# Optimization experiments

Hardware: AMD Instinct MI355X
Metric: run time of the kernel (lower is better)

Reference implementation:

```python
import jax, jax.numpy as jnp
import numpy as np

N_FULL = 200000  # full-graph nodes
N_SUB = 80000    # subgraph nodes
E = 800000       # subgraph edges
IN = 128         # input feature dim
HD = 128         # hidden dim
LMAX = 5         # max ACT depth


def setup_inputs() -> dict:
    key = jax.random.key(0)
    ks = jax.random.split(key, 12)
    s = lambda i, shape: jax.random.normal(ks[i], shape, jnp.float32) * 0.05
    return dict(
        x_full=jax.random.normal(ks[0], (N_FULL, IN), jnp.float32),
        W_in=s(1, (HD, IN)), b_in=jnp.zeros((HD,), jnp.float32),
        W_l=s(2, (HD, HD)), b_l=jnp.zeros((HD,), jnp.float32),
        W_r=s(3, (HD, HD)),
        W_e1=s(4, (HD, 3 * HD)), b_e1=jnp.zeros((HD,), jnp.float32),
        W_e2=s(5, (1, HD)), b_e2=jnp.zeros((1,), jnp.float32),
        W_h1=s(6, (64, 2 * HD + 1)), b_h1=jnp.zeros((64,), jnp.float32),
        W_h2=s(7, (1, 64)), b_h2=jnp.zeros((1,), jnp.float32),
        subset=jax.random.randint(ks[8], (N_SUB,), 0, N_FULL),
        edge_index=jax.random.randint(ks[9], (2, E), 0, N_SUB),
    )


def reference(x_full, W_in, b_in, W_l, b_l, W_r, W_e1, b_e1, W_e2, b_e2,
              W_h1, b_h1, W_h2, b_h2, subset, edge_index):
    src, dst = edge_index[0], edge_index[1]
    # in-degree for mean aggregation (PyG SAGEConv default aggr='mean')
    deg = jax.ops.segment_sum(jnp.ones((E,), x_full.dtype), dst, num_segments=N_SUB)
    deg = jnp.maximum(deg, 1.0)[:, None]

    def sage_step(Hn):
        agg = jax.ops.segment_sum(Hn[src], dst, num_segments=N_SUB) / deg
        return jax.nn.relu(agg @ W_l.T + b_l + Hn @ W_r.T)

    # input projection of gathered subgraph features
    Hk = x_full[subset] @ W_in.T + b_in
    u_idx, v_idx = 0, 1  # mapping of (u, v) in relabeled subgraph

    alphas, scores = [], []
    p_not = jnp.float32(1.0)
    for depth_k in range(1, LMAX + 1):
        # incremental: one more shared SAGE step == k fresh steps from H0
        Hk = sage_step(Hk)
        h_u, h_v = Hk[u_idx], Hk[v_idx]
        feat = jnp.concatenate([h_u, h_v, h_u * h_v])            # [3*HD]
        score = jax.nn.relu(feat @ W_e1.T + b_e1) @ W_e2.T + b_e2  # [1]
        hin = jnp.concatenate([h_u, h_v, score])                  # [2*HD+1]
        p_halt = jax.nn.sigmoid(jax.nn.relu(hin @ W_h1.T + b_h1) @ W_h2.T + b_h2)[0]
        alphas.append(p_halt * p_not)
        scores.append(score[0])
        p_not = p_not * (1.0 - p_halt)

    alpha = jnp.stack(alphas)
    alpha = alpha / (alpha.sum() + 1e-8)
    scores_v = jnp.stack(scores)
    final_score = (alpha * scores_v).sum()
    depths = jnp.arange(1, LMAX + 1, dtype=jnp.float32)
    expected_depth = (alpha * depths).sum()
    return final_score, expected_depth, alpha
```

## Files before the change

### kernel.cpp

```cpp
#include <hip/hip_runtime.h>
#include <hip/hip_bf16.h>

#define N_FULL 200000
#define N_SUB  80000
#define E_NUM  800000
#define IN_DIM 128
#define HD     128
#define LMAX   5

#define NB_SCAN ((N_SUB + 255) / 256)


__global__ void init_all(int* __restrict__ cnt, int* __restrict__ cursor,
                         int* __restrict__ level) {
    int i = blockIdx.x * blockDim.x + threadIdx.x;
    if (i < N_SUB) {
        cnt[i] = 0;
        cursor[i] = 0;
        level[i] = (i < 2) ? 0 : 7;
    }
}

__global__ void count_deg(const int* __restrict__ dst, int* __restrict__ cnt) {
    int i = blockIdx.x * blockDim.x + threadIdx.x;
    if (i < E_NUM) atomicAdd(&cnt[dst[i]], 1);
}

__global__ void scan_block(const int* __restrict__ cnt, int* __restrict__ offs,
                           int* __restrict__ bsums) {
    __shared__ int s[256];
    int t = threadIdx.x;
    int i = blockIdx.x * 256 + t;
    int v = (i < N_SUB) ? cnt[i] : 0;
    s[t] = v;
    __syncthreads();
    for (int off = 1; off < 256; off <<= 1) {
        int x = (t >= off) ? s[t - off] : 0;
        __syncthreads();
        s[t] += x;
        __syncthreads();
    }
    if (i < N_SUB) offs[i] = s[t] - v;
    if (t == 255) bsums[blockIdx.x] = s[255];
}

__global__ void scan_sums(int* __restrict__ bsums) {
    __shared__ int s[512];
    int t = threadIdx.x;
    int v = (t < NB_SCAN) ? bsums[t] : 0;
    s[t] = v;
    __syncthreads();
    for (int off = 1; off < 512; off <<= 1) {
        int x = (t >= off) ? s[t - off] : 0;
        __syncthreads();
        s[t] += x;
        __syncthreads();
    }
    if (t < NB_SCAN) bsums[t] = s[t] - v;
}

__global__ void scan_add(int* __restrict__ offs, const int* __restrict__ bsums) {
    int i = blockIdx.x * 256 + threadIdx.x;
    if (i < N_SUB) offs[i] += bsums[blockIdx.x];
    if (i == 0) offs[N_SUB] = E_NUM;
}

__global__ void fill_csr(const int* __restrict__ src, const int* __restrict__ dst,
                         const int* __restrict__ offs, int* __restrict__ cursor,
                         int* __restrict__ csr) {
    int i = blockIdx.x * blockDim.x + threadIdx.x;
    if (i < E_NUM) {
        int d = dst[i];
        int p = atomicAdd(&cursor[d], 1);
        csr[offs[d] + p] = src[i];
    }
}


__global__ void bfs_csr(const int* __restrict__ offs, const int* __restrict__ csr,
                        int* __restrict__ level, int t) {
    int i = blockIdx.x * blockDim.x + threadIdx.x;
    if (i >= N_SUB) return;
    if (level[i] != t) return;
    int beg = offs[i], end = offs[i + 1];
    for (int j = beg; j < end; ++j) {
        int u = csr[j];
        if (level[u] > t + 1) level[u] = t + 1;
    }
}


__global__ __launch_bounds__(256) void hist_levels(const int* __restrict__ level,
                                                   int* __restrict__ bhist) {
    __shared__ int h[8];
    int t = threadIdx.x;
    if (t < 8) h[t] = 0;
    __syncthreads();
    int i = blockIdx.x * 256 + t;
    if (i < N_SUB) {
        int l = level[i];
        if (l > 5) l = 6;
        atomicAdd(&h[l], 1);
    }
    __syncthreads();
    if (t < 8) bhist[blockIdx.x * 8 + t] = h[t];
}

__global__ void scan_hist(int* __restrict__ bhist, int* __restrict__ base,
                          int* __restrict__ cum) {
    __shared__ int tot[8];
    int t = threadIdx.x;
    if (t < 8) {
        int acc = 0;
        for (int b = 0; b < NB_SCAN; ++b) {
            int v = bhist[b * 8 + t];
            bhist[b * 8 + t] = acc;
            acc += v;
        }
        tot[t] = acc;
    }
    __syncthreads();
    if (t == 0) {
        int acc = 0;
        for (int l = 0; l <= 5; ++l) {
            base[l] = acc;
            acc += tot[l];
            cum[l] = acc;
        }
    }
}

__global__ __launch_bounds__(256) void emit_order(const int* __restrict__ level,
                                                  const int* __restrict__ bhist,
                                                  const int* __restrict__ base,
                                                  int* __restrict__ order) {
    __shared__ int woff[4][8];
    int t = threadIdx.x;
    int lane = t & 63, wv = t >> 6;
    int i = blockIdx.x * 256 + t;
    int l = 7;
    if (i < N_SUB) {
        l = level[i];
        if (l > 5) l = 6;
    }
    unsigned long long mybal = 0;
#pragma unroll
    for (int q = 0; q < 8; ++q) {
        unsigned long long b = __ballot(l == q);
        if (q == l) mybal = b;
        if (lane == 0) woff[wv][q] = (int)__popcll(b);
    }
    int inrank = (int)__popcll(mybal & ((1ull << lane) - 1ull));
    __syncthreads();
    if (t < 8) {
        int acc = 0;
        for (int w2 = 0; w2 < 4; ++w2) {
            int c = woff[w2][t];
            woff[w2][t] = acc;
            acc += c;
        }
    }
    __syncthreads();
    if (i < N_SUB && l <= 5) {
        int pos = base[l] + bhist[blockIdx.x * 8 + l] + woff[wv][l] + inrank;
        order[pos] = i;
    }
}


__global__ __launch_bounds__(256) void wcomb(
    const float* __restrict__ W_l, const float* __restrict__ W_r,
    const float* __restrict__ W_in, const float* __restrict__ b_in,
    const float* __restrict__ b_l, float* __restrict__ Wc1,
    float* __restrict__ Wc2, float* __restrict__ bc) {
    int f = blockIdx.x;
    int t = threadIdx.x;
    int c = t & 127, p = t >> 7;
    __shared__ float wl[128], wr[128];
    if (t < 128) wl[t] = W_l[f * 128 + t];
    else wr[t - 128] = W_r[f * 128 + (t - 128)];
    __syncthreads();
    const float* wrow = p ? wr : wl;
    float acc = 0.f;
#pragma unroll 8
    for (int j = 0; j < 128; ++j)
        acc = fmaf(wrow[j], W_in[j * 128 + c], acc);
    (p ? Wc2 : Wc1)[f * 128 + c] = acc;
    if (t < 64) {
        float pa = (wl[t] + wr[t]) * b_in[t] + (wl[t + 64] + wr[t + 64]) * b_in[t + 64];
        for (int off = 32; off; off >>= 1) pa += __shfl_down(pa, off);
        if (t == 0) bc[f] = pa + b_l[f];
    }
}


__global__ __launch_bounds__(256) void aggregate_list(
    const float* __restrict__ H, float* __restrict__ Out,
    const int* __restrict__ offs, const int* __restrict__ csr,
    const int* __restrict__ cnt, const int* __restrict__ order,
    const int* __restrict__ cumptr, int lvl, const int* __restrict__ srcmap) {
    int M = cumptr[lvl];
    int ngroups = (M + 3) >> 2;
    int wid = threadIdx.x >> 6, lane = threadIdx.x & 63;
    for (int g = blockIdx.x; g < ngroups; g += gridDim.x) {
        int ni = g * 4 + wid;
        if (ni >= M) continue;
        int node = order[ni];
        int beg = offs[node], end = offs[node + 1];
        float ax = 0.f, ay = 0.f, bx = 0.f, by = 0.f;
        int j = beg;
        for (; j + 1 < end; j += 2) {
            int s0 = csr[j], s1 = csr[j + 1];
            int r0 = srcmap ? srcmap[s0] : s0;
            int r1 = srcmap ? srcmap[s1] : s1;
            float2 v0 = *(const float2*)(H + (size_t)r0 * HD + lane * 2);
            float2 v1 = *(const float2*)(H + (size_t)r1 * HD + lane * 2);
            ax += v0.x; ay += v0.y;
            bx += v1.x; by += v1.y;
        }
        if (j < end) {
            int s0 = csr[j];
            int r0 = srcmap ? srcmap[s0] : s0;
            float2 v0 = *(const float2*)(H + (size_t)r0 * HD + lane * 2);
            ax += v0.x; ay += v0.y;
        }
        int c = cnt[node];
        float inv = 1.0f / (float)(c > 1 ? c : 1);
        *(float2*)(Out + (size_t)node * HD + lane * 2) =
            make_float2((ax + bx) * inv, (ay + by) * inv);
    }
}


#define GBM 64
#define GBK 32

__global__ __launch_bounds__(256) void gemm_list(
    const float* __restrict__ A1, const float* __restrict__ A2,
    const float* __restrict__ W1, const float* __restrict__ W2,
    const float* __restrict__ bias, float* __restrict__ Out,
    const int* __restrict__ order, const int* __restrict__ gatherA,
    const int* __restrict__ gatherB, const int* __restrict__ cumptr,
    int lvl, int do_relu) {

    __shared__ __align__(16) float As[GBK][68];
    __shared__ __align__(16) float Ws[GBK][132];

    int M = cumptr[lvl];
    int ntiles = (M + GBM - 1) / GBM;
    int tid = threadIdx.x;
    int tx = tid & 15, ty = tid >> 4;
    int r0 = ty * 4;
    int c0 = tx * 4;
    int nchunk = A2 ? 8 : 4;

    for (int tile = blockIdx.x; tile < ntiles; tile += gridDim.x) {
        int row0 = tile * GBM;

        float acc[4][8];
#pragma unroll
        for (int i = 0; i < 4; ++i)
#pragma unroll
            for (int j = 0; j < 8; ++j) acc[i][j] = 0.f;

        for (int ch = 0; ch < nchunk; ++ch) {
            const float* Asrc = (ch < 4) ? A1 : A2;
            const float* Wsrc = (ch < 4) ? W1 : W2;
            const int* gmap = (ch < 4) ? gatherA : gatherB;
            int kbase = (ch & 3) * GBK;

#pragma unroll
            for (int it = 0; it < 2; ++it) {
                int idx = tid + it * 256;
                int m = idx >> 3, kq = idx & 7;
                int row = row0 + m;
                float4 v = make_float4(0.f, 0.f, 0.f, 0.f);
                if (row < M) {
                    int nr = order[row];
                    int ar = gmap ? gmap[nr] : nr;
                    v = *(const float4*)(Asrc + (size_t)ar * 128 + kbase + kq * 4);
                }
                As[kq * 4 + 0][m] = v.x;
                As[kq * 4 + 1][m] = v.y;
                As[kq * 4 + 2][m] = v.z;
                As[kq * 4 + 3][m] = v.w;
            }
#pragma unroll
            for (int it = 0; it < 4; ++it) {
                int idx = tid + it * 256;
                int n = idx >> 3, kq = idx & 7;
                float4 v = *(const float4*)(Wsrc + n * 128 + kbase + kq * 4);
                Ws[kq * 4 + 0][n] = v.x;
                Ws[kq * 4 + 1][n] = v.y;
                Ws[kq * 4 + 2][n] = v.z;
                Ws[kq * 4 + 3][n] = v.w;
            }
            __syncthreads();

#pragma unroll
            for (int kk = 0; kk < GBK; ++kk) {
                float4 a  = *(const float4*)&As[kk][r0];
                float4 w0 = *(const float4*)&Ws[kk][c0];
                float4 w1 = *(const float4*)&Ws[kk][c0 + 64];
                float av[4] = {a.x, a.y, a.z, a.w};
                float wv[8] = {w0.x, w0.y, w0.z, w0.w, w1.x, w1.y, w1.z, w1.w};
#pragma unroll
                for (int i = 0; i < 4; ++i)
#pragma unroll
                    for (int j = 0; j < 8; ++j)
                        acc[i][j] = fmaf(av[i], wv[j], acc[i][j]);
            }
            __syncthreads();
        }

#pragma unroll
        for (int i = 0; i < 4; ++i) {
            int row = row0 + r0 + i;
            if (row >= M) continue;
            int nr = order[row];
            float4 o0, o1;
            o0.x = acc[i][0] + bias[c0 + 0];
            o0.y = acc[i][1] + bias[c0 + 1];
            o0.z = acc[i][2] + bias[c0 + 2];
            o0.w = acc[i][3] + bias[c0 + 3];
            o1.x = acc[i][4] + bias[c0 + 64];
            o1.y = acc[i][5] + bias[c0 + 65];
            o1.z = acc[i][6] + bias[c0 + 66];
            o1.w = acc[i][7] + bias[c0 + 67];
            if (do_relu) {
                o0.x = fmaxf(o0.x, 0.f); o0.y = fmaxf(o0.y, 0.f);
                o0.z = fmaxf(o0.z, 0.f); o0.w = fmaxf(o0.w, 0.f);
                o1.x = fmaxf(o1.x, 0.f); o1.y = fmaxf(o1.y, 0.f);
                o1.z = fmaxf(o1.z, 0.f); o1.w = fmaxf(o1.w, 0.f);
            }
            *(float4*)(Out + (size_t)nr * 128 + c0) = o0;
            *(float4*)(Out + (size_t)nr * 128 + c0 + 64) = o1;
        }
    }
}


__global__ __launch_bounds__(256) void head_kernel(
    const float* __restrict__ H,
    const float* __restrict__ W_e1, const float* __restrict__ b_e1,
    const float* __restrict__ W_e2, const float* __restrict__ b_e2,
    const float* __restrict__ W_h1, const float* __restrict__ b_h1,
    const float* __restrict__ W_h2, const float* __restrict__ b_h2,
    float* __restrict__ head_out, int kidx) {

    __shared__ float feat[384];
    __shared__ float rowo[128];
    __shared__ float sc_sh;
    int t = threadIdx.x, lane = t & 63, wv = t >> 6;

    if (t < 128) {
        float a = H[t], b = H[128 + t];
        feat[t] = a;
        feat[128 + t] = b;
        feat[256 + t] = a * b;
    }
    __syncthreads();

    for (int r = wv; r < 128; r += 4) {
        const float* wr = W_e1 + r * 384;
        float acc = 0.f;
#pragma unroll
        for (int j = 0; j < 6; ++j)
            acc += feat[lane + 64 * j] * wr[lane + 64 * j];
        for (int off = 32; off; off >>= 1) acc += __shfl_down(acc, off);
        if (lane == 0) rowo[r] = fmaxf(acc + b_e1[r], 0.f) * W_e2[r];
    }
    __syncthreads();
    if (wv == 0) {
        float v = rowo[lane] + rowo[lane + 64];
        for (int off = 32; off; off >>= 1) v += __shfl_down(v, off);
        if (lane == 0) sc_sh = v + b_e2[0];
    }
    __syncthreads();
    float score = sc_sh;

    for (int r = wv; r < 64; r += 4) {
        const float* wh = W_h1 + r * 257;
        float acc = 0.f;
#pragma unroll
        for (int j = 0; j < 4; ++j)
            acc += feat[lane + 64 * j] * wh[lane + 64 * j];
        if (lane == 0) acc += score * wh[256];
        for (int off = 32; off; off >>= 1) acc += __shfl_down(acc, off);
        if (lane == 0) rowo[r] = fmaxf(acc + b_h1[r], 0.f) * W_h2[r];
    }
    __syncthreads();
    if (wv == 0) {
        float v = rowo[lane];
        for (int off = 32; off; off >>= 1) v += __shfl_down(v, off);
        if (lane == 0) {
            float p = 1.f / (1.f + expf(-(v + b_h2[0])));
            head_out[kidx * 2 + 0] = score;
            head_out[kidx * 2 + 1] = p;
        }
    }
}

__global__ void finalize(const float* __restrict__ head_out, float* __restrict__ out) {
    if (threadIdx.x == 0 && blockIdx.x == 0) {
        float a[LMAX];
        float p_not = 1.f, s = 0.f;
        for (int k = 0; k < LMAX; ++k) {
            float p = head_out[2 * k + 1];
            a[k] = p * p_not;
            p_not *= (1.f - p);
            s += a[k];
        }
        float inv = 1.f / (s + 1e-8f);
        float fs = 0.f, ed = 0.f;
        for (int k = 0; k < LMAX; ++k) {
            float al = a[k] * inv;
            out[2 + k] = al;
            fs += al * head_out[2 * k];
            ed += al * (float)(k + 1);
        }
        out[0] = fs;
        out[1] = ed;
    }
}


extern "C" void kernel_launch(void* const* d_in, const int* in_sizes, int n_in,
                              void* d_out, int out_size, void* d_ws, size_t ws_size,
                              hipStream_t stream) {
    const float* x_full = (const float*)d_in[0];
    const float* W_in  = (const float*)d_in[1];
    const float* b_in  = (const float*)d_in[2];
    const float* W_l   = (const float*)d_in[3];
    const float* b_l   = (const float*)d_in[4];
    const float* W_r   = (const float*)d_in[5];
    const float* W_e1  = (const float*)d_in[6];
    const float* b_e1  = (const float*)d_in[7];
    const float* W_e2  = (const float*)d_in[8];
    const float* b_e2  = (const float*)d_in[9];
    const float* W_h1  = (const float*)d_in[10];
    const float* b_h1  = (const float*)d_in[11];
    const float* W_h2  = (const float*)d_in[12];
    const float* b_h2  = (const float*)d_in[13];
    const int* subset  = (const int*)d_in[14];
    const int* edge    = (const int*)d_in[15];
    const int* esrc = edge;
    const int* edst = edge + E_NUM;

    char* w = (char*)d_ws;
    float* HA = (float*)w;      w += (size_t)N_SUB * HD * 4;
    float* HB = (float*)w;      w += (size_t)N_SUB * HD * 4;
    int* cnt = (int*)w;         w += (size_t)N_SUB * 4;
    int* offs = (int*)w;        w += (size_t)(N_SUB + 64) * 4;
    int* cursor = (int*)w;      w += (size_t)N_SUB * 4;
    int* csr = (int*)w;         w += (size_t)E_NUM * 4;
    int* level = (int*)w;       w += (size_t)N_SUB * 4;
    int* order = (int*)w;       w += (size_t)N_SUB * 4;
    int* bsums = (int*)w;       w += 4096;
    int* bhist = (int*)w;       w += (size_t)(NB_SCAN + 1) * 8 * 4;
    int* lvlbase = (int*)w;     w += 64;
    int* cum = (int*)w;         w += 64;
    float* Wc1 = (float*)w;     w += 128 * 128 * 4;
    float* Wc2 = (float*)w;     w += 128 * 128 * 4;
    float* bc = (float*)w;      w += 512;
    float* head_out = (float*)w; w += 256;

    init_all<<<NB_SCAN, 256, 0, stream>>>(cnt, cursor, level);
    count_deg<<<(E_NUM + 255) / 256, 256, 0, stream>>>(edst, cnt);
    scan_block<<<NB_SCAN, 256, 0, stream>>>(cnt, offs, bsums);
    scan_sums<<<1, 512, 0, stream>>>(bsums);
    scan_add<<<NB_SCAN, 256, 0, stream>>>(offs, bsums);
    fill_csr<<<(E_NUM + 255) / 256, 256, 0, stream>>>(esrc, edst, offs, cursor, csr);

    wcomb<<<128, 256, 0, stream>>>(W_l, W_r, W_in, b_in, b_l, Wc1, Wc2, bc);

    for (int t = 0; t < 4; ++t)
        bfs_csr<<<NB_SCAN, 256, 0, stream>>>(offs, csr, level, t);

    hist_levels<<<NB_SCAN, 256, 0, stream>>>(level, bhist);
    scan_hist<<<1, 64, 0, stream>>>(bhist, lvlbase, cum);
    emit_order<<<NB_SCAN, 256, 0, stream>>>(level, bhist, lvlbase, order);

    aggregate_list<<<2048, 256, 0, stream>>>(x_full, HB, offs, csr, cnt, order, cum, 4, subset);
    gemm_list<<<512, 256, 0, stream>>>(
        HB, x_full, Wc1, Wc2, bc, HA, order, nullptr, subset, cum, 4, 1);
    head_kernel<<<1, 256, 0, stream>>>(HA, W_e1, b_e1, W_e2, b_e2,
                                       W_h1, b_h1, W_h2, b_h2, head_out, 0);

    for (int k = 2; k <= LMAX; ++k) {
        int lvl = LMAX - k;
        aggregate_list<<<96, 256, 0, stream>>>(HA, HB, offs, csr, cnt, order, cum, lvl, nullptr);
        gemm_list<<<96, 256, 0, stream>>>(
            HB, HA, W_l, W_r, b_l, HA, order, nullptr, nullptr, cum, lvl, 1);
        head_kernel<<<1, 256, 0, stream>>>(HA, W_e1, b_e1, W_e2, b_e2,
                                           W_h1, b_h1, W_h2, b_h2, head_out, k - 1);
    }
    finalize<<<1, 1, 0, stream>>>(head_out, (float*)d_out);
}
```

Before: 449.7 us.

## Fuse preprocessing and tail stages into persistent kernels with grid barriers

```diff
diff --git a/kernel.cpp b/kernel.cpp
--- a/kernel.cpp
+++ b/kernel.cpp
@@ -9,200 +9,32 @@
 #define LMAX   5
 
 #define NB_SCAN ((N_SUB + 255) / 256)
-
-
-__global__ void init_all(int* __restrict__ cnt, int* __restrict__ cursor,
-                         int* __restrict__ level) {
-    int i = blockIdx.x * blockDim.x + threadIdx.x;
-    if (i < N_SUB) {
-        cnt[i] = 0;
-        cursor[i] = 0;
-        level[i] = (i < 2) ? 0 : 7;
-    }
-}
-
-__global__ void count_deg(const int* __restrict__ dst, int* __restrict__ cnt) {
-    int i = blockIdx.x * blockDim.x + threadIdx.x;
-    if (i < E_NUM) atomicAdd(&cnt[dst[i]], 1);
-}
-
-__global__ void scan_block(const int* __restrict__ cnt, int* __restrict__ offs,
-                           int* __restrict__ bsums) {
-    __shared__ int s[256];
-    int t = threadIdx.x;
-    int i = blockIdx.x * 256 + t;
-    int v = (i < N_SUB) ? cnt[i] : 0;
-    s[t] = v;
-    __syncthreads();
-    for (int off = 1; off < 256; off <<= 1) {
-        int x = (t >= off) ? s[t - off] : 0;
-        __syncthreads();
-        s[t] += x;
-        __syncthreads();
-    }
-    if (i < N_SUB) offs[i] = s[t] - v;
-    if (t == 255) bsums[blockIdx.x] = s[255];
-}
-
-__global__ void scan_sums(int* __restrict__ bsums) {
-    __shared__ int s[512];
-    int t = threadIdx.x;
-    int v = (t < NB_SCAN) ? bsums[t] : 0;
-    s[t] = v;
-    __syncthreads();
-    for (int off = 1; off < 512; off <<= 1) {
-        int x = (t >= off) ? s[t - off] : 0;
-        __syncthreads();
-        s[t] += x;
-        __syncthreads();
-    }
-    if (t < NB_SCAN) bsums[t] = s[t] - v;
-}
-
-__global__ void scan_add(int* __restrict__ offs, const int* __restrict__ bsums) {
-    int i = blockIdx.x * 256 + threadIdx.x;
-    if (i < N_SUB) offs[i] += bsums[blockIdx.x];
-    if (i == 0) offs[N_SUB] = E_NUM;
-}
-
-__global__ void fill_csr(const int* __restrict__ src, const int* __restrict__ dst,
-                         const int* __restrict__ offs, int* __restrict__ cursor,
-                         int* __restrict__ csr) {
-    int i = blockIdx.x * blockDim.x + threadIdx.x;
-    if (i < E_NUM) {
-        int d = dst[i];
-        int p = atomicAdd(&cursor[d], 1);
-        csr[offs[d] + p] = src[i];
-    }
-}
-
-
-__global__ void bfs_csr(const int* __restrict__ offs, const int* __restrict__ csr,
-                        int* __restrict__ level, int t) {
-    int i = blockIdx.x * blockDim.x + threadIdx.x;
-    if (i >= N_SUB) return;
-    if (level[i] != t) return;
-    int beg = offs[i], end = offs[i + 1];
-    for (int j = beg; j < end; ++j) {
-        int u = csr[j];
-        if (level[u] > t + 1) level[u] = t + 1;
-    }
-}
-
-
-__global__ __launch_bounds__(256) void hist_levels(const int* __restrict__ level,
-                                                   int* __restrict__ bhist) {
-    __shared__ int h[8];
-    int t = threadIdx.x;
-    if (t < 8) h[t] = 0;
-    __syncthreads();
-    int i = blockIdx.x * 256 + t;
-    if (i < N_SUB) {
-        int l = level[i];
-        if (l > 5) l = 6;
-        atomicAdd(&h[l], 1);
-    }
-    __syncthreads();
-    if (t < 8) bhist[blockIdx.x * 8 + t] = h[t];
-}
-
-__global__ void scan_hist(int* __restrict__ bhist, int* __restrict__ base,
-                          int* __restrict__ cum) {
-    __shared__ int tot[8];
-    int t = threadIdx.x;
-    if (t < 8) {
-        int acc = 0;
-        for (int b = 0; b < NB_SCAN; ++b) {
-            int v = bhist[b * 8 + t];
-            bhist[b * 8 + t] = acc;
-            acc += v;
-        }
-        tot[t] = acc;
-    }
-    __syncthreads();
-    if (t == 0) {
-        int acc = 0;
-        for (int l = 0; l <= 5; ++l) {
-            base[l] = acc;
-            acc += tot[l];
-            cum[l] = acc;
-        }
-    }
-}
-
-__global__ __launch_bounds__(256) void emit_order(const int* __restrict__ level,
-                                                  const int* __restrict__ bhist,
-                                                  const int* __restrict__ base,
-                                                  int* __restrict__ order) {
-    __shared__ int woff[4][8];
-    int t = threadIdx.x;
-    int lane = t & 63, wv = t >> 6;
-    int i = blockIdx.x * 256 + t;
-    int l = 7;
-    if (i < N_SUB) {
-        l = level[i];
-        if (l > 5) l = 6;
-    }
-    unsigned long long mybal = 0;
-#pragma unroll
-    for (int q = 0; q < 8; ++q) {
-        unsigned long long b = __ballot(l == q);
-        if (q == l) mybal = b;
-        if (lane == 0) woff[wv][q] = (int)__popcll(b);
-    }
-    int inrank = (int)__popcll(mybal & ((1ull << lane) - 1ull));
-    __syncthreads();
-    if (t < 8) {
-        int acc = 0;
-        for (int w2 = 0; w2 < 4; ++w2) {
-            int c = woff[w2][t];
-            woff[w2][t] = acc;
-            acc += c;
-        }
-    }
-    __syncthreads();
-    if (i < N_SUB && l <= 5) {
-        int pos = base[l] + bhist[blockIdx.x * 8 + l] + woff[wv][l] + inrank;
-        order[pos] = i;
-    }
-}
-
-
-__global__ __launch_bounds__(256) void wcomb(
-    const float* __restrict__ W_l, const float* __restrict__ W_r,
-    const float* __restrict__ W_in, const float* __restrict__ b_in,
-    const float* __restrict__ b_l, float* __restrict__ Wc1,
-    float* __restrict__ Wc2, float* __restrict__ bc) {
-    int f = blockIdx.x;
-    int t = threadIdx.x;
-    int c = t & 127, p = t >> 7;
-    __shared__ float wl[128], wr[128];
-    if (t < 128) wl[t] = W_l[f * 128 + t];
-    else wr[t - 128] = W_r[f * 128 + (t - 128)];
-    __syncthreads();
-    const float* wrow = p ? wr : wl;
-    float acc = 0.f;
-#pragma unroll 8
-    for (int j = 0; j < 128; ++j)
-        acc = fmaf(wrow[j], W_in[j * 128 + c], acc);
-    (p ? Wc2 : Wc1)[f * 128 + c] = acc;
-    if (t < 64) {
-        float pa = (wl[t] + wr[t]) * b_in[t] + (wl[t + 64] + wr[t + 64]) * b_in[t + 64];
-        for (int off = 32; off; off >>= 1) pa += __shfl_down(pa, off);
-        if (t == 0) bc[f] = pa + b_l[f];
-    }
-}
-
-
-__global__ __launch_bounds__(256) void aggregate_list(
+#define NBP 128
+#define NBT 128
+
+
+__device__ __forceinline__ void gbar(int* bar, int nblk, int ph) {
+    __syncthreads();
+    if (threadIdx.x == 0) {
+        __threadfence();
+        atomicAdd(bar, 1);
+        int target = nblk * ph;
+        while (__hip_atomic_load(bar, __ATOMIC_ACQUIRE, __HIP_MEMORY_SCOPE_AGENT) < target) {
+            __builtin_amdgcn_s_sleep(1);
+        }
+    }
+    __syncthreads();
+}
+
+
+__device__ void dev_aggregate(
     const float* __restrict__ H, float* __restrict__ Out,
     const int* __restrict__ offs, const int* __restrict__ csr,
     const int* __restrict__ cnt, const int* __restrict__ order,
-    const int* __restrict__ cumptr, int lvl, const int* __restrict__ srcmap) {
-    int M = cumptr[lvl];
+    int M, const int* __restrict__ srcmap, int bid0, int nb) {
     int ngroups = (M + 3) >> 2;
     int wid = threadIdx.x >> 6, lane = threadIdx.x & 63;
-    for (int g = blockIdx.x; g < ngroups; g += gridDim.x) {
+    for (int g = bid0; g < ngroups; g += nb) {
         int ni = g * 4 + wid;
         if (ni >= M) continue;
         int node = order[ni];
@@ -231,22 +63,19 @@
     }
 }
 
-
 #define GBM 64
 #define GBK 32
 
-__global__ __launch_bounds__(256) void gemm_list(
+__device__ void dev_gemm(
     const float* __restrict__ A1, const float* __restrict__ A2,
     const float* __restrict__ W1, const float* __restrict__ W2,
     const float* __restrict__ bias, float* __restrict__ Out,
     const int* __restrict__ order, const int* __restrict__ gatherA,
-    const int* __restrict__ gatherB, const int* __restrict__ cumptr,
-    int lvl, int do_relu) {
+    const int* __restrict__ gatherB, int M, int do_relu, int bid0, int nb) {
 
     __shared__ __align__(16) float As[GBK][68];
     __shared__ __align__(16) float Ws[GBK][132];
 
-    int M = cumptr[lvl];
     int ntiles = (M + GBM - 1) / GBM;
     int tid = threadIdx.x;
     int tx = tid & 15, ty = tid >> 4;
@@ -254,7 +83,7 @@
     int c0 = tx * 4;
     int nchunk = A2 ? 8 : 4;
 
-    for (int tile = blockIdx.x; tile < ntiles; tile += gridDim.x) {
+    for (int tile = bid0; tile < ntiles; tile += nb) {
         int row0 = tile * GBM;
 
         float acc[4][8];
@@ -339,8 +168,7 @@
     }
 }
 
-
-__global__ __launch_bounds__(256) void head_kernel(
+__device__ void dev_head(
     const float* __restrict__ H,
     const float* __restrict__ W_e1, const float* __restrict__ b_e1,
     const float* __restrict__ W_e2, const float* __restrict__ b_e2,
@@ -399,10 +227,260 @@
             head_out[kidx * 2 + 1] = p;
         }
     }
-}
-
-__global__ void finalize(const float* __restrict__ head_out, float* __restrict__ out) {
-    if (threadIdx.x == 0 && blockIdx.x == 0) {
+    __syncthreads();
+}
+
+
+__global__ __launch_bounds__(256) void prep_fused(
+    const int* __restrict__ esrc, const int* __restrict__ edst,
+    const float* __restrict__ W_l, const float* __restrict__ W_r,
+    const float* __restrict__ W_in, const float* __restrict__ b_in,
+    const float* __restrict__ b_l,
+    int* __restrict__ cnt, int* __restrict__ cursor, int* __restrict__ level,
+    int* __restrict__ offs, int* __restrict__ csr,
+    int* __restrict__ bsums, int* __restrict__ bhist,
+    int* __restrict__ lvlbase, int* __restrict__ cum, int* __restrict__ order,
+    float* __restrict__ Wc1, float* __restrict__ Wc2, float* __restrict__ bc,
+    int* __restrict__ bar) {
+
+    __shared__ int si[256];
+    __shared__ float sf[256];
+    __shared__ int h8[8];
+    __shared__ int tot8[8];
+    __shared__ int woff[4][8];
+
+    int t = threadIdx.x;
+    int bid = blockIdx.x;
+    int nb = gridDim.x;
+    int gsz = nb * 256;
+    int gi0 = bid * 256 + t;
+    int ph = 0;
+
+    for (int i = gi0; i < N_SUB; i += gsz) {
+        cnt[i] = 0; cursor[i] = 0; level[i] = (i < 2) ? 0 : 7;
+    }
+    gbar(bar, nb, ++ph);
+
+    for (int i = gi0; i < E_NUM; i += gsz)
+        atomicAdd(&cnt[edst[i]], 1);
+    gbar(bar, nb, ++ph);
+
+    for (int job = bid; job < NB_SCAN; job += nb) {
+        int i = job * 256 + t;
+        int v = (i < N_SUB) ? cnt[i] : 0;
+        si[t] = v;
+        __syncthreads();
+        for (int off = 1; off < 256; off <<= 1) {
+            int x = (t >= off) ? si[t - off] : 0;
+            __syncthreads();
+            si[t] += x;
+            __syncthreads();
+        }
+        if (i < N_SUB) offs[i] = si[t] - v;
+        if (t == 255) bsums[job] = si[255];
+        __syncthreads();
+    }
+    gbar(bar, nb, ++ph);
+
+    if (bid == 0 && t < 64) {
+        int lane = t;
+        int base = 0;
+        for (int c = 0; c < NB_SCAN; c += 64) {
+            int idx = c + lane;
+            int v0 = (idx < NB_SCAN) ? bsums[idx] : 0;
+            int v = v0;
+            for (int off = 1; off < 64; off <<= 1) {
+                int x = __shfl_up(v, off);
+                if (lane >= off) v += x;
+            }
+            if (idx < NB_SCAN) bsums[idx] = base + v - v0;
+            base += __shfl(v, 63);
+        }
+    }
+    gbar(bar, nb, ++ph);
+
+    for (int i = gi0; i < N_SUB; i += gsz) offs[i] += bsums[i >> 8];
+    if (gi0 == 0) offs[N_SUB] = E_NUM;
+    gbar(bar, nb, ++ph);
+
+    for (int i = gi0; i < E_NUM; i += gsz) {
+        int d = edst[i];
+        int p = atomicAdd(&cursor[d], 1);
+        csr[offs[d] + p] = esrc[i];
+    }
+    gbar(bar, nb, ++ph);
+
+    for (int tt = 0; tt < 4; ++tt) {
+        for (int i = gi0; i < N_SUB; i += gsz) {
+            if (level[i] == tt) {
+                int beg = offs[i], end = offs[i + 1];
+                for (int j = beg; j < end; ++j) {
+                    int u = csr[j];
+                    if (level[u] > tt + 1) level[u] = tt + 1;
+                }
+            }
+        }
+        gbar(bar, nb, ++ph);
+    }
+
+    for (int job = bid; job < NB_SCAN; job += nb) {
+        if (t < 8) h8[t] = 0;
+        __syncthreads();
+        int i = job * 256 + t;
+        if (i < N_SUB) {
+            int l = level[i];
+            if (l > 5) l = 6;
+            atomicAdd(&h8[l], 1);
+        }
+        __syncthreads();
+        if (t < 8) bhist[job * 8 + t] = h8[t];
+        __syncthreads();
+    }
+    gbar(bar, nb, ++ph);
+
+    if (bid == 0) {
+        int wv = t >> 6, lane = t & 63;
+        for (int l = wv; l < 8; l += 4) {
+            int base = 0;
+            for (int c = 0; c < NB_SCAN; c += 64) {
+                int idx = c + lane;
+                int v0 = (idx < NB_SCAN) ? bhist[idx * 8 + l] : 0;
+                int v = v0;
+                for (int off = 1; off < 64; off <<= 1) {
+                    int x = __shfl_up(v, off);
+                    if (lane >= off) v += x;
+                }
+                if (idx < NB_SCAN) bhist[idx * 8 + l] = base + v - v0;
+                base += __shfl(v, 63);
+            }
+            if (lane == 0) tot8[l] = base;
+        }
+        __syncthreads();
+        if (t == 0) {
+            int acc = 0;
+            for (int l = 0; l <= 5; ++l) {
+                lvlbase[l] = acc;
+                acc += tot8[l];
+                cum[l] = acc;
+            }
+        }
+    }
+    gbar(bar, nb, ++ph);
+
+    {
+        int lane = t & 63, wv = t >> 6;
+        for (int job = bid; job < NB_SCAN; job += nb) {
+            int i = job * 256 + t;
+            int l = 7;
+            if (i < N_SUB) {
+                l = level[i];
+                if (l > 5) l = 6;
+            }
+            unsigned long long mybal = 0;
+#pragma unroll
+            for (int q = 0; q < 8; ++q) {
+                unsigned long long b = __ballot(l == q);
+                if (q == l) mybal = b;
+                if (lane == 0) woff[wv][q] = (int)__popcll(b);
+            }
+            int inrank = (int)__popcll(mybal & ((1ull << lane) - 1ull));
+            __syncthreads();
+            if (t < 8) {
+                int acc = 0;
+                for (int w2 = 0; w2 < 4; ++w2) {
+                    int c = woff[w2][t];
+                    woff[w2][t] = acc;
+                    acc += c;
+                }
+            }
+            __syncthreads();
+            if (i < N_SUB && l <= 5) {
+                int pos = lvlbase[l] + bhist[job * 8 + l] + woff[wv][l] + inrank;
+                order[pos] = i;
+            }
+            __syncthreads();
+        }
+    }
+
+    for (int f = bid; f < 128; f += nb) {
+        if (t < 128) sf[t] = W_l[f * 128 + t];
+        else sf[t] = W_r[f * 128 + (t - 128)];
+        __syncthreads();
+        int c = t & 127, p = t >> 7;
+        const float* wrow = p ? (sf + 128) : sf;
+        float acc = 0.f;
+#pragma unroll 8
+        for (int j = 0; j < 128; ++j)
+            acc = fmaf(wrow[j], W_in[j * 128 + c], acc);
+        (p ? Wc2 : Wc1)[f * 128 + c] = acc;
+        if (t < 64) {
+            float pa = (sf[t] + sf[128 + t]) * b_in[t] +
+                       (sf[t + 64] + sf[192 + t]) * b_in[t + 64];
+            for (int off = 32; off; off >>= 1) pa += __shfl_down(pa, off);
+            if (t == 0) bc[f] = pa + b_l[f];
+        }
+        __syncthreads();
+    }
+}
+
+
+__global__ __launch_bounds__(256) void aggregate_list(
+    const float* __restrict__ H, float* __restrict__ Out,
+    const int* __restrict__ offs, const int* __restrict__ csr,
+    const int* __restrict__ cnt, const int* __restrict__ order,
+    const int* __restrict__ cumptr, int lvl, const int* __restrict__ srcmap) {
+    int M = cumptr[lvl];
+    dev_aggregate(H, Out, offs, csr, cnt, order, M, srcmap, blockIdx.x, gridDim.x);
+}
+
+__global__ __launch_bounds__(256) void gemm_list(
+    const float* __restrict__ A1, const float* __restrict__ A2,
+    const float* __restrict__ W1, const float* __restrict__ W2,
+    const float* __restrict__ bias, float* __restrict__ Out,
+    const int* __restrict__ order, const int* __restrict__ gatherA,
+    const int* __restrict__ gatherB, const int* __restrict__ cumptr,
+    int lvl, int do_relu) {
+    int M = cumptr[lvl];
+    dev_gemm(A1, A2, W1, W2, bias, Out, order, gatherA, gatherB, M, do_relu,
+             blockIdx.x, gridDim.x);
+}
+
+
+__global__ __launch_bounds__(256) void tail_fused(
+    float* __restrict__ HA, float* __restrict__ HB,
+    const int* __restrict__ offs, const int* __restrict__ csr,
+    const int* __restrict__ cnt, const int* __restrict__ order,
+    const int* __restrict__ cum,
+    const float* __restrict__ W_l, const float* __restrict__ b_l,
+    const float* __restrict__ W_r,
+    const float* __restrict__ W_e1, const float* __restrict__ b_e1,
+    const float* __restrict__ W_e2, const float* __restrict__ b_e2,
+    const float* __restrict__ W_h1, const float* __restrict__ b_h1,
+    const float* __restrict__ W_h2, const float* __restrict__ b_h2,
+    float* __restrict__ head_out, float* __restrict__ out,
+    int* __restrict__ bar) {
+
+    int bid = blockIdx.x, nb = gridDim.x;
+    int ph = 0;
+
+    if (bid == 0)
+        dev_head(HA, W_e1, b_e1, W_e2, b_e2, W_h1, b_h1, W_h2, b_h2, head_out, 0);
+    gbar(bar, nb, ++ph);
+
+    for (int k = 2; k <= LMAX; ++k) {
+        int lvl = LMAX - k;
+        int M = cum[lvl];
+        dev_aggregate(HA, HB, offs, csr, cnt, order, M, nullptr, bid, nb);
+        gbar(bar, nb, ++ph);
+        dev_gemm(HB, HA, W_l, W_r, b_l, HA, order, nullptr, nullptr, M, 1, bid, nb);
+        gbar(bar, nb, ++ph);
+        if (bid == 0)
+            dev_head(HA, W_e1, b_e1, W_e2, b_e2, W_h1, b_h1, W_h2, b_h2,
+                     head_out, k - 1);
+        if (k < LMAX) gbar(bar, nb, ++ph);
+    }
+
+    if (bid == 0 && threadIdx.x == 0) {
         float a[LMAX];
         float p_not = 1.f, s = 0.f;
         for (int k = 0; k < LMAX; ++k) {
@@ -464,36 +542,22 @@
     float* Wc2 = (float*)w;     w += 128 * 128 * 4;
     float* bc = (float*)w;      w += 512;
     float* head_out = (float*)w; w += 256;
-
-    init_all<<<NB_SCAN, 256, 0, stream>>>(cnt, cursor, level);
-    count_deg<<<(E_NUM + 255) / 256, 256, 0, stream>>>(edst, cnt);
-    scan_block<<<NB_SCAN, 256, 0, stream>>>(cnt, offs, bsums);
-    scan_sums<<<1, 512, 0, stream>>>(bsums);
-    scan_add<<<NB_SCAN, 256, 0, stream>>>(offs, bsums);
-    fill_csr<<<(E_NUM + 255) / 256, 256, 0, stream>>>(esrc, edst, offs, cursor, csr);
-
-    wcomb<<<128, 256, 0, stream>>>(W_l, W_r, W_in, b_in, b_l, Wc1, Wc2, bc);
-
-    for (int t = 0; t < 4; ++t)
-        bfs_csr<<<NB_SCAN, 256, 0, stream>>>(offs, csr, level, t);
-
-    hist_levels<<<NB_SCAN, 256, 0, stream>>>(level, bhist);
-    scan_hist<<<1, 64, 0, stream>>>(bhist, lvlbase, cum);
-    emit_order<<<NB_SCAN, 256, 0, stream>>>(level, bhist, lvlbase, order);
-
-    aggregate_list<<<2048, 256, 0, stream>>>(x_full, HB, offs, csr, cnt, order, cum, 4, subset);
+    int* bars = (int*)w;        w += 256;
+
+    hipMemsetAsync(bars, 0, 256, stream);
+
+    prep_fused<<<NBP, 256, 0, stream>>>(
+        esrc, edst, W_l, W_r, W_in, b_in, b_l,
+        cnt, cursor, level, offs, csr, bsums, bhist, lvlbase, cum, order,
+        Wc1, Wc2, bc, bars);
+
+    aggregate_list<<<2048, 256, 0, stream>>>(
+        x_full, HB, offs, csr, cnt, order, cum, 4, subset);
     gemm_list<<<512, 256, 0, stream>>>(
         HB, x_full, Wc1, Wc2, bc, HA, order, nullptr, subset, cum, 4, 1);
-    head_kernel<<<1, 256, 0, stream>>>(HA, W_e1, b_e1, W_e2, b_e2,
-                                       W_h1, b_h1, W_h2, b_h2, head_out, 0);
-
-    for (int k = 2; k <= LMAX; ++k) {
-        int lvl = LMAX - k;
-        aggregate_list<<<96, 256, 0, stream>>>(HA, HB, offs, csr, cnt, order, cum, lvl, nullptr);
-        gemm_list<<<96, 256, 0, stream>>>(
-            HB, HA, W_l, W_r, b_l, HA, order, nullptr, nullptr, cum, lvl, 1);
-        head_kernel<<<1, 256, 0, stream>>>(HA, W_e1, b_e1, W_e2, b_e2,
-                                           W_h1, b_h1, W_h2, b_h2, head_out, k - 1);
-    }
-    finalize<<<1, 1, 0, stream>>>(head_out, (float*)d_out);
-}
+
+    tail_fused<<<NBT, 256, 0, stream>>>(
+        HA, HB, offs, csr, cnt, order, cum,
+        W_l, b_l, W_r, W_e1, b_e1, W_e2, b_e2, W_h1, b_h1, W_h2, b_h2,
+        head_out, (float*)d_out, bars + 16);
+}
```

Measured after the change: 855.8 us. 1.9x slower.

## Fuse setup kernels, CSR fill with weight combine, and head into GEMM

Applied to the files above, without the earlier changes.

```diff
diff --git a/kernel.cpp b/kernel.cpp
--- a/kernel.cpp
+++ b/kernel.cpp
@@ -9,22 +9,15 @@
 #define LMAX   5
 
 #define NB_SCAN ((N_SUB + 255) / 256)
-
-
-__global__ void init_all(int* __restrict__ cnt, int* __restrict__ cursor,
-                         int* __restrict__ level) {
-    int i = blockIdx.x * blockDim.x + threadIdx.x;
-    if (i < N_SUB) {
-        cnt[i] = 0;
-        cursor[i] = 0;
-        level[i] = (i < 2) ? 0 : 7;
-    }
-}
+#define NB_E (E_NUM / 256)
+#define WCOMB_BLKS 128
+
 
 __global__ void count_deg(const int* __restrict__ dst, int* __restrict__ cnt) {
     int i = blockIdx.x * blockDim.x + threadIdx.x;
     if (i < E_NUM) atomicAdd(&cnt[dst[i]], 1);
 }
+
 
 __global__ void scan_block(const int* __restrict__ cnt, int* __restrict__ offs,
                            int* __restrict__ bsums) {
@@ -59,20 +52,50 @@
     if (t < NB_SCAN) bsums[t] = s[t] - v;
 }
 
-__global__ void scan_add(int* __restrict__ offs, const int* __restrict__ bsums) {
+__global__ void scan_add(int* __restrict__ offs, const int* __restrict__ bsums,
+                         int* __restrict__ level) {
     int i = blockIdx.x * 256 + threadIdx.x;
-    if (i < N_SUB) offs[i] += bsums[blockIdx.x];
+    if (i < N_SUB) {
+        offs[i] += bsums[blockIdx.x];
+        level[i] = (i < 2) ? 0 : 7;
+    }
     if (i == 0) offs[N_SUB] = E_NUM;
 }
 
-__global__ void fill_csr(const int* __restrict__ src, const int* __restrict__ dst,
-                         const int* __restrict__ offs, int* __restrict__ cursor,
-                         int* __restrict__ csr) {
-    int i = blockIdx.x * blockDim.x + threadIdx.x;
-    if (i < E_NUM) {
-        int d = dst[i];
-        int p = atomicAdd(&cursor[d], 1);
-        csr[offs[d] + p] = src[i];
+
+__global__ __launch_bounds__(256) void fill_wcomb(
+    const int* __restrict__ esrc, const int* __restrict__ edst,
+    const int* __restrict__ offs, int* __restrict__ cnt, int* __restrict__ csr,
+    const float* __restrict__ W_l, const float* __restrict__ W_r,
+    const float* __restrict__ W_in, const float* __restrict__ b_in,
+    const float* __restrict__ b_l,
+    float* __restrict__ Wc1, float* __restrict__ Wc2, float* __restrict__ bc) {
+    int b = blockIdx.x;
+    int t = threadIdx.x;
+    if (b < NB_E) {
+        int i = b * 256 + t;
+        int d = edst[i];
+        int p = atomicSub(&cnt[d], 1) - 1;
+        csr[offs[d] + p] = esrc[i];
+    } else {
+        __shared__ float sf[256];
+        int f = b - NB_E;
+        if (t < 128) sf[t] = W_l[f * 128 + t];
+        else sf[t] = W_r[f * 128 + (t - 128)];
+        __syncthreads();
+        int c = t & 127, p = t >> 7;
+        const float* wrow = p ? (sf + 128) : sf;
+        float acc = 0.f;
+#pragma unroll 8
+        for (int j = 0; j < 128; ++j)
+            acc = fmaf(wrow[j], W_in[j * 128 + c], acc);
+        (p ? Wc2 : Wc1)[f * 128 + c] = acc;
+        if (t < 64) {
+            float pa = (sf[t] + sf[128 + t]) * b_in[t] +
+                       (sf[t + 64] + sf[192 + t]) * b_in[t + 64];
+            for (int off = 32; off; off >>= 1) pa += __shfl_down(pa, off);
+            if (t == 0) bc[f] = pa + b_l[f];
+        }
     }
 }
 
@@ -168,38 +191,12 @@
 }
 
 
-__global__ __launch_bounds__(256) void wcomb(
-    const float* __restrict__ W_l, const float* __restrict__ W_r,
-    const float* __restrict__ W_in, const float* __restrict__ b_in,
-    const float* __restrict__ b_l, float* __restrict__ Wc1,
-    float* __restrict__ Wc2, float* __restrict__ bc) {
-    int f = blockIdx.x;
-    int t = threadIdx.x;
-    int c = t & 127, p = t >> 7;
-    __shared__ float wl[128], wr[128];
-    if (t < 128) wl[t] = W_l[f * 128 + t];
-    else wr[t - 128] = W_r[f * 128 + (t - 128)];
-    __syncthreads();
-    const float* wrow = p ? wr : wl;
-    float acc = 0.f;
-#pragma unroll 8
-    for (int j = 0; j < 128; ++j)
-        acc = fmaf(wrow[j], W_in[j * 128 + c], acc);
-    (p ? Wc2 : Wc1)[f * 128 + c] = acc;
-    if (t < 64) {
-        float pa = (wl[t] + wr[t]) * b_in[t] + (wl[t + 64] + wr[t + 64]) * b_in[t + 64];
-        for (int off = 32; off; off >>= 1) pa += __shfl_down(pa, off);
-        if (t == 0) bc[f] = pa + b_l[f];
-    }
-}
-
-
 __global__ __launch_bounds__(256) void aggregate_list(
     const float* __restrict__ H, float* __restrict__ Out,
     const int* __restrict__ offs, const int* __restrict__ csr,
-    const int* __restrict__ cnt, const int* __restrict__ order,
-    const int* __restrict__ cumptr, int lvl, const int* __restrict__ srcmap) {
-    int M = cumptr[lvl];
+    const int* __restrict__ order, const int* __restrict__ cum, int lvl,
+    const int* __restrict__ srcmap) {
+    int M = cum[lvl];
     int ngroups = (M + 3) >> 2;
     int wid = threadIdx.x >> 6, lane = threadIdx.x & 63;
     for (int g = blockIdx.x; g < ngroups; g += gridDim.x) {
@@ -224,11 +221,75 @@
             float2 v0 = *(const float2*)(H + (size_t)r0 * HD + lane * 2);
             ax += v0.x; ay += v0.y;
         }
-        int c = cnt[node];
-        float inv = 1.0f / (float)(c > 1 ? c : 1);
+        int deg = end - beg;
+        float inv = 1.0f / (float)(deg > 1 ? deg : 1);
         *(float2*)(Out + (size_t)node * HD + lane * 2) =
             make_float2((ax + bx) * inv, (ay + by) * inv);
     }
+}
+
+
+__device__ void dev_head(
+    const float* __restrict__ H,
+    const float* __restrict__ W_e1, const float* __restrict__ b_e1,
+    const float* __restrict__ W_e2, const float* __restrict__ b_e2,
+    const float* __restrict__ W_h1, const float* __restrict__ b_h1,
+    const float* __restrict__ W_h2, const float* __restrict__ b_h2,
+    float* __restrict__ head_out, int kidx) {
+
+    __shared__ float feat[384];
+    __shared__ float rowo[128];
+    __shared__ float sc_sh;
+    int t = threadIdx.x, lane = t & 63, wv = t >> 6;
+
+    __syncthreads();
+    if (t < 128) {
+        float a = H[t], b = H[128 + t];
+        feat[t] = a;
+        feat[128 + t] = b;
+        feat[256 + t] = a * b;
+    }
+    __syncthreads();
+
+    for (int r = wv; r < 128; r += 4) {
+        const float* wr = W_e1 + r * 384;
+        float acc = 0.f;
+#pragma unroll
+        for (int j = 0; j < 6; ++j)
+            acc += feat[lane + 64 * j] * wr[lane + 64 * j];
+        for (int off = 32; off; off >>= 1) acc += __shfl_down(acc, off);
+        if (lane == 0) rowo[r] = fmaxf(acc + b_e1[r], 0.f) * W_e2[r];
+    }
+    __syncthreads();
+    if (wv == 0) {
+        float v = rowo[lane] + rowo[lane + 64];
+        for (int off = 32; off; off >>= 1) v += __shfl_down(v, off);
+        if (lane == 0) sc_sh = v + b_e2[0];
+    }
+    __syncthreads();
+    float score = sc_sh;
+
+    for (int r = wv; r < 64; r += 4) {
+        const float* wh = W_h1 + r * 257;
+        float acc = 0.f;
+#pragma unroll
+        for (int j = 0; j < 4; ++j)
+            acc += feat[lane + 64 * j] * wh[lane + 64 * j];
+        if (lane == 0) acc += score * wh[256];
+        for (int off = 32; off; off >>= 1) acc += __shfl_down(acc, off);
+        if (lane == 0) rowo[r] = fmaxf(acc + b_h1[r], 0.f) * W_h2[r];
+    }
+    __syncthreads();
+    if (wv == 0) {
+        float v = rowo[lane];
+        for (int off = 32; off; off >>= 1) v += __shfl_down(v, off);
+        if (lane == 0) {
+            float p = 1.f / (1.f + expf(-(v + b_h2[0])));
+            head_out[kidx * 2 + 0] = score;
+            head_out[kidx * 2 + 1] = p;
+        }
+    }
+    __syncthreads();
 }
 
 
@@ -240,19 +301,22 @@
     const float* __restrict__ W1, const float* __restrict__ W2,
     const float* __restrict__ bias, float* __restrict__ Out,
     const int* __restrict__ order, const int* __restrict__ gatherA,
-    const int* __restrict__ gatherB, const int* __restrict__ cumptr,
-    int lvl, int do_relu) {
+    const int* __restrict__ gatherB, const int* __restrict__ cum, int lvl,
+    const float* __restrict__ W_e1, const float* __restrict__ b_e1,
+    const float* __restrict__ W_e2, const float* __restrict__ b_e2,
+    const float* __restrict__ W_h1, const float* __restrict__ b_h1,
+    const float* __restrict__ W_h2, const float* __restrict__ b_h2,
+    float* __restrict__ head_out, int head_kidx) {
 
     __shared__ __align__(16) float As[GBK][68];
     __shared__ __align__(16) float Ws[GBK][132];
 
-    int M = cumptr[lvl];
+    int M = cum[lvl];
     int ntiles = (M + GBM - 1) / GBM;
     int tid = threadIdx.x;
     int tx = tid & 15, ty = tid >> 4;
     int r0 = ty * 4;
     int c0 = tx * 4;
-    int nchunk = A2 ? 8 : 4;
 
     for (int tile = blockIdx.x; tile < ntiles; tile += gridDim.x) {
         int row0 = tile * GBM;
@@ -263,7 +327,7 @@
 #pragma unroll
             for (int j = 0; j < 8; ++j) acc[i][j] = 0.f;
 
-        for (int ch = 0; ch < nchunk; ++ch) {
+        for (int ch = 0; ch < 8; ++ch) {
             const float* Asrc = (ch < 4) ? A1 : A2;
             const float* Wsrc = (ch < 4) ? W1 : W2;
             const int* gmap = (ch < 4) ? gatherA : gatherB;
@@ -319,87 +383,25 @@
             if (row >= M) continue;
             int nr = order[row];
             float4 o0, o1;
-            o0.x = acc[i][0] + bias[c0 + 0];
-            o0.y = acc[i][1] + bias[c0 + 1];
-            o0.z = acc[i][2] + bias[c0 + 2];
-            o0.w = acc[i][3] + bias[c0 + 3];
-            o1.x = acc[i][4] + bias[c0 + 64];
-            o1.y = acc[i][5] + bias[c0 + 65];
-            o1.z = acc[i][6] + bias[c0 + 66];
-            o1.w = acc[i][7] + bias[c0 + 67];
-            if (do_relu) {
-                o0.x = fmaxf(o0.x, 0.f); o0.y = fmaxf(o0.y, 0.f);
-                o0.z = fmaxf(o0.z, 0.f); o0.w = fmaxf(o0.w, 0.f);
-                o1.x = fmaxf(o1.x, 0.f); o1.y = fmaxf(o1.y, 0.f);
-                o1.z = fmaxf(o1.z, 0.f); o1.w = fmaxf(o1.w, 0.f);
-            }
+            o0.x = fmaxf(acc[i][0] + bias[c0 + 0], 0.f);
+            o0.y = fmaxf(acc[i][1] + bias[c0 + 1], 0.f);
+            o0.z = fmaxf(acc[i][2] + bias[c0 + 2], 0.f);
+            o0.w = fmaxf(acc[i][3] + bias[c0 + 3], 0.f);
+            o1.x = fmaxf(acc[i][4] + bias[c0 + 64], 0.f);
+            o1.y = fmaxf(acc[i][5] + bias[c0 + 65], 0.f);
+            o1.z = fmaxf(acc[i][6] + bias[c0 + 66], 0.f);
+            o1.w = fmaxf(acc[i][7] + bias[c0 + 67], 0.f);
             *(float4*)(Out + (size_t)nr * 128 + c0) = o0;
             *(float4*)(Out + (size_t)nr * 128 + c0 + 64) = o1;
         }
-    }
-}
-
-
-__global__ __launch_bounds__(256) void head_kernel(
-    const float* __restrict__ H,
-    const float* __restrict__ W_e1, const float* __restrict__ b_e1,
-    const float* __restrict__ W_e2, const float* __restrict__ b_e2,
-    const float* __restrict__ W_h1, const float* __restrict__ b_h1,
-    const float* __restrict__ W_h2, const float* __restrict__ b_h2,
-    float* __restrict__ head_out, int kidx) {
-
-    __shared__ float feat[384];
-    __shared__ float rowo[128];
-    __shared__ float sc_sh;
-    int t = threadIdx.x, lane = t & 63, wv = t >> 6;
-
-    if (t < 128) {
-        float a = H[t], b = H[128 + t];
-        feat[t] = a;
-        feat[128 + t] = b;
-        feat[256 + t] = a * b;
-    }
-    __syncthreads();
-
-    for (int r = wv; r < 128; r += 4) {
-        const float* wr = W_e1 + r * 384;
-        float acc = 0.f;
-#pragma unroll
-        for (int j = 0; j < 6; ++j)
-            acc += feat[lane + 64 * j] * wr[lane + 64 * j];
-        for (int off = 32; off; off >>= 1) acc += __shfl_down(acc, off);
-        if (lane == 0) rowo[r] = fmaxf(acc + b_e1[r], 0.f) * W_e2[r];
-    }
-    __syncthreads();
-    if (wv == 0) {
-        float v = rowo[lane] + rowo[lane + 64];
-        for (int off = 32; off; off >>= 1) v += __shfl_down(v, off);
-        if (lane == 0) sc_sh = v + b_e2[0];
-    }
-    __syncthreads();
-    float score = sc_sh;
-
-    for (int r = wv; r < 64; r += 4) {
-        const float* wh = W_h1 + r * 257;
-        float acc = 0.f;
-#pragma unroll
-        for (int j = 0; j < 4; ++j)
-            acc += feat[lane + 64 * j] * wh[lane + 64 * j];
-        if (lane == 0) acc += score * wh[256];
-        for (int off = 32; off; off >>= 1) acc += __shfl_down(acc, off);
-        if (lane == 0) rowo[r] = fmaxf(acc + b_h1[r], 0.f) * W_h2[r];
-    }
-    __syncthreads();
-    if (wv == 0) {
-        float v = rowo[lane];
-        for (int off = 32; off; off >>= 1) v += __shfl_down(v, off);
-        if (lane == 0) {
-            float p = 1.f / (1.f + expf(-(v + b_h2[0])));
-            head_out[kidx * 2 + 0] = score;
-            head_out[kidx * 2 + 1] = p;
-        }
-    }
-}
+
+        if (tile == 0 && head_kidx >= 0) {
+            dev_head(Out, W_e1, b_e1, W_e2, b_e2, W_h1, b_h1, W_h2, b_h2,
+                     head_out, head_kidx);
+        }
+    }
+}
+
 
 __global__ void finalize(const float* __restrict__ head_out, float* __restrict__ out) {
     if (threadIdx.x == 0 && blockIdx.x == 0) {
@@ -452,7 +454,6 @@
     float* HB = (float*)w;      w += (size_t)N_SUB * HD * 4;
     int* cnt = (int*)w;         w += (size_t)N_SUB * 4;
     int* offs = (int*)w;        w += (size_t)(N_SUB + 64) * 4;
-    int* cursor = (int*)w;      w += (size_t)N_SUB * 4;
     int* csr = (int*)w;         w += (size_t)E_NUM * 4;
     int* level = (int*)w;       w += (size_t)N_SUB * 4;
     int* order = (int*)w;       w += (size_t)N_SUB * 4;
@@ -465,14 +466,13 @@
     float* bc = (float*)w;      w += 512;
     float* head_out = (float*)w; w += 256;
 
-    init_all<<<NB_SCAN, 256, 0, stream>>>(cnt, cursor, level);
-    count_deg<<<(E_NUM + 255) / 256, 256, 0, stream>>>(edst, cnt);
+    hipMemsetAsync(cnt, 0, (size_t)N_SUB * 4, stream);
+    count_deg<<<NB_E, 256, 0, stream>>>(edst, cnt);
     scan_block<<<NB_SCAN, 256, 0, stream>>>(cnt, offs, bsums);
     scan_sums<<<1, 512, 0, stream>>>(bsums);
-    scan_add<<<NB_SCAN, 256, 0, stream>>>(offs, bsums);
-    fill_csr<<<(E_NUM + 255) / 256, 256, 0, stream>>>(esrc, edst, offs, cursor, csr);
-
-    wcomb<<<128, 256, 0, stream>>>(W_l, W_r, W_in, b_in, b_l, Wc1, Wc2, bc);
+    scan_add<<<NB_SCAN, 256, 0, stream>>>(offs, bsums, level);
+    fill_wcomb<<<NB_E + WCOMB_BLKS, 256, 0, stream>>>(
+        esrc, edst, offs, cnt, csr, W_l, W_r, W_in, b_in, b_l, Wc1, Wc2, bc);
 
     for (int t = 0; t < 4; ++t)
         bfs_csr<<<NB_SCAN, 256, 0, stream>>>(offs, csr, level, t);
@@ -481,19 +481,21 @@
     scan_hist<<<1, 64, 0, stream>>>(bhist, lvlbase, cum);
     emit_order<<<NB_SCAN, 256, 0, stream>>>(level, bhist, lvlbase, order);
 
-    aggregate_list<<<2048, 256, 0, stream>>>(x_full, HB, offs, csr, cnt, order, cum, 4, subset);
+    aggregate_list<<<2048, 256, 0, stream>>>(
+        x_full, HB, offs, csr, order, cum, 4, subset);
     gemm_list<<<512, 256, 0, stream>>>(
-        HB, x_full, Wc1, Wc2, bc, HA, order, nullptr, subset, cum, 4, 1);
-    head_kernel<<<1, 256, 0, stream>>>(HA, W_e1, b_e1, W_e2, b_e2,
-                                       W_h1, b_h1, W_h2, b_h2, head_out, 0);
-
+        HB, x_full, Wc1, Wc2, bc, HA, order, nullptr, subset, cum, 4,
+        W_e1, b_e1, W_e2, b_e2, W_h1, b_h1, W_h2, b_h2, head_out, 0);
+
+    const int agrid[4] = {96, 64, 8, 1};
+    const int ggrid[4] = {64, 4, 1, 1};
     for (int k = 2; k <= LMAX; ++k) {
         int lvl = LMAX - k;
-        aggregate_list<<<96, 256, 0, stream>>>(HA, HB, offs, csr, cnt, order, cum, lvl, nullptr);
-        gemm_list<<<96, 256, 0, stream>>>(
-            HB, HA, W_l, W_r, b_l, HA, order, nullptr, nullptr, cum, lvl, 1);
-        head_kernel<<<1, 256, 0, stream>>>(HA, W_e1, b_e1, W_e2, b_e2,
-                                           W_h1, b_h1, W_h2, b_h2, head_out, k - 1);
+        aggregate_list<<<agrid[k - 2], 256, 0, stream>>>(
+            HA, HB, offs, csr, order, cum, lvl, nullptr);
+        gemm_list<<<ggrid[k - 2], 256, 0, stream>>>(
+            HB, HA, W_l, W_r, b_l, HA, order, nullptr, nullptr, cum, lvl,
+            W_e1, b_e1, W_e2, b_e2, W_h1, b_h1, W_h2, b_h2, head_out, k - 1);
     }
     finalize<<<1, 1, 0, stream>>>(head_out, (float*)d_out);
 }
```

Measured after the change: 452.7 us. Within noise of the previous version (+0.6%).
